# Kernel optimization log

Hardware: AMD Instinct MI355X
Metric: run time of the kernel (lower is better)

## Reference

```python
import jax, jax.numpy as jnp
import numpy as np

VOCAB, EMB, HID, OUT = 50000, 512, 1024, 4
B, T = 128, 256


def setup_inputs() -> dict:
    key = jax.random.key(0)
    ks = jax.random.split(key, 12)
    std0 = 1.0 / np.sqrt(HID)
    u = lambda k, shp, s: jax.random.uniform(k, shp, jnp.float32, -s, s)
    return {
        "fx": jax.random.randint(ks[0], (B, T), 0, VOCAB),
        "emb": jax.random.normal(ks[1], (VOCAB, EMB), jnp.float32),
        "x2h_w0": u(ks[2], (HID, EMB), std0),
        "x2h_b0": u(ks[3], (HID,), std0),
        "h2h_w0": u(ks[4], (HID, HID), std0),
        "h2h_b0": u(ks[5], (HID,), std0),
        "x2h_w1": u(ks[6], (HID, HID), std0),
        "x2h_b1": u(ks[7], (HID,), std0),
        "h2h_w1": u(ks[8], (HID, HID), std0),
        "h2h_b1": u(ks[9], (HID,), std0),
        "fc_w": u(ks[10], (OUT, HID), 1.0 / np.sqrt(HID)),
        "fc_b": u(ks[11], (OUT,), 1.0 / np.sqrt(HID)),
    }


def reference(fx, emb, x2h_w0, x2h_b0, h2h_w0, h2h_b0,
              x2h_w1, x2h_b1, h2h_w1, h2h_b1, fc_w, fc_b):
    x = emb[fx]                      # [B, T, EMB]
    xT = jnp.swapaxes(x, 0, 1)       # [T, B, EMB] for scan over time
    h0 = jnp.zeros((fx.shape[0], HID), jnp.float32)
    h1 = jnp.zeros((fx.shape[0], HID), jnp.float32)

    def step(carry, xt):
        h0, h1 = carry
        # layer 0: tanh(x2h(x_t) + h2h(h0))
        h0 = jnp.tanh(xt @ x2h_w0.T + x2h_b0 + h0 @ h2h_w0.T + h2h_b0)
        # layer 1 consumes the freshly-updated layer-0 hidden (as in the torch loop)
        h1 = jnp.tanh(h0 @ x2h_w1.T + x2h_b1 + h1 @ h2h_w1.T + h2h_b1)
        return (h0, h1), None

    (h0, h1), _ = jax.lax.scan(step, (h0, h1), xT)
    # fc applied to last timestep's top-layer hidden (outs[-1])
    return h1 @ fc_w.T + fc_b        # [B, OUT]
```

## Files before the change

kernel.cpp:

```cpp
#include <hip/hip_runtime.h>
#include <hip/hip_bf16.h>

#define HID   1024
#define EMB   512
#define BATCH 128
#define TT    256
#define OUTN  4
#define BH    (BATCH * HID)

typedef short bf16x8 __attribute__((ext_vector_type(8)));
typedef float f32x4  __attribute__((ext_vector_type(4)));
typedef int   i32x4  __attribute__((ext_vector_type(4)));

__device__ __forceinline__ float bf2f(unsigned short h) {
    return __uint_as_float(((unsigned)h) << 16);
}
__device__ __forceinline__ unsigned short f2bf(float f) {
    unsigned u = __float_as_uint(f);
    u += 0x7FFFu + ((u >> 16) & 1u);
    return (unsigned short)(u >> 16);
}
__device__ __forceinline__ void cvt8(const float* s, unsigned short* d) {
    float4 a = *(const float4*)s, b = *(const float4*)(s + 4);
    unsigned short t[8] = {f2bf(a.x), f2bf(a.y), f2bf(a.z), f2bf(a.w),
                           f2bf(b.x), f2bf(b.y), f2bf(b.z), f2bf(b.w)};
    *(int4*)d = *(const int4*)t;
}
__device__ __forceinline__ bf16x8 pack8(const float* s) {
    float4 a = *(const float4*)s, b = *(const float4*)(s + 4);
    bf16x8 f;
    f[0] = (short)f2bf(a.x); f[1] = (short)f2bf(a.y);
    f[2] = (short)f2bf(a.z); f[3] = (short)f2bf(a.w);
    f[4] = (short)f2bf(b.x); f[5] = (short)f2bf(b.y);
    f[6] = (short)f2bf(b.z); f[7] = (short)f2bf(b.w);
    return f;
}

__global__ __launch_bounds__(256) void wcvt_kernel(
    const float* __restrict__ w, unsigned short* __restrict__ o)
{
    const int i = (blockIdx.x * 256 + threadIdx.x) * 8;
    cvt8(w + i, o + i);
}

__global__ __launch_bounds__(256) void prefx_kernel(
    const int* __restrict__ fx, const float* __restrict__ emb,
    const unsigned short* __restrict__ wx0b, const float* __restrict__ bx0,
    const float* __restrict__ bh0, unsigned short* __restrict__ pre0)
{
    __shared__ __align__(16) unsigned short A[64 * 520];
    const int mtile = blockIdx.x >> 2;
    const int ntile = blockIdx.x & 3;
    const int tid = threadIdx.x;

    {
        const int row = tid >> 2, part = tid & 3;
        const int r = mtile * 64 + row;
        const int t = r >> 7, b = r & 127;
        const int v = fx[b * TT + t];
        const float* src = emb + (size_t)v * EMB + part * 128;
        unsigned short* dst = A + row * 520 + part * 128;
        #pragma unroll
        for (int i = 0; i < 128; i += 8) cvt8(src + i, dst + i);
    }
    __syncthreads();

    const int wave = tid >> 6, lane = tid & 63, q = lane >> 4, nl = lane & 15;
    const int col0 = ntile * 256 + wave * 64;

    f32x4 acc[4][4] = {};
    for (int kc = 0; kc < 16; ++kc) {
        bf16x8 bfr[4], afr[4];
        #pragma unroll
        for (int nt = 0; nt < 4; ++nt)
            bfr[nt] = *(const bf16x8*)(wx0b + (size_t)(col0 + nt * 16 + nl) * EMB + kc * 32 + q * 8);
        #pragma unroll
        for (int mt = 0; mt < 4; ++mt)
            afr[mt] = *(const bf16x8*)(A + (mt * 16 + nl) * 520 + kc * 32 + q * 8);
        #pragma unroll
        for (int mt = 0; mt < 4; ++mt)
            #pragma unroll
            for (int nt = 0; nt < 4; ++nt)
                acc[mt][nt] = __builtin_amdgcn_mfma_f32_16x16x32_bf16(afr[mt], bfr[nt], acc[mt][nt], 0, 0, 0);
    }

    #pragma unroll
    for (int nt = 0; nt < 4; ++nt) {
        const int gc = col0 + nt * 16 + nl;
        const float bias = bx0[gc] + bh0[gc];
        #pragma unroll
        for (int mt = 0; mt < 4; ++mt)
            #pragma unroll
            for (int r = 0; r < 4; ++r) {
                const int grow = mtile * 64 + mt * 16 + q * 4 + r;
                pre0[(size_t)grow * HID + gc] = f2bf(acc[mt][nt][r] + bias);
            }
    }
}

__device__ __forceinline__ void bypass_store16B(unsigned short* dst, i32x4 v) {
    asm volatile("global_store_dwordx4 %0, %1, off sc0 sc1\n\t"
                 "s_waitcnt vmcnt(0)"
                 :: "v"(dst), "v"(v) : "memory");
}

__device__ __forceinline__ void bypass_load8A(const unsigned short* p2, bf16x8 A[8]) {
    asm volatile(
        "global_load_dwordx4 %0, %8, off sc0 sc1\n\t"
        "global_load_dwordx4 %1, %8, off offset:64 sc0 sc1\n\t"
        "global_load_dwordx4 %2, %8, off offset:128 sc0 sc1\n\t"
        "global_load_dwordx4 %3, %8, off offset:192 sc0 sc1\n\t"
        "global_load_dwordx4 %4, %8, off offset:256 sc0 sc1\n\t"
        "global_load_dwordx4 %5, %8, off offset:320 sc0 sc1\n\t"
        "global_load_dwordx4 %6, %8, off offset:384 sc0 sc1\n\t"
        "global_load_dwordx4 %7, %8, off offset:448 sc0 sc1\n\t"
        "s_waitcnt vmcnt(0)"
        : "=&v"(A[0]), "=&v"(A[1]), "=&v"(A[2]), "=&v"(A[3]),
          "=&v"(A[4]), "=&v"(A[5]), "=&v"(A[6]), "=&v"(A[7])
        : "v"(p2) : "memory");
}

__device__ __forceinline__ void bypass_ld8_seq(const unsigned short* p, bf16x8 r[8]) {
    asm volatile(
        "global_load_dwordx4 %0, %8, off sc0 sc1\n\t"
        "global_load_dwordx4 %1, %8, off offset:16 sc0 sc1\n\t"
        "global_load_dwordx4 %2, %8, off offset:32 sc0 sc1\n\t"
        "global_load_dwordx4 %3, %8, off offset:48 sc0 sc1\n\t"
        "global_load_dwordx4 %4, %8, off offset:64 sc0 sc1\n\t"
        "global_load_dwordx4 %5, %8, off offset:80 sc0 sc1\n\t"
        "global_load_dwordx4 %6, %8, off offset:96 sc0 sc1\n\t"
        "global_load_dwordx4 %7, %8, off offset:112 sc0 sc1\n\t"
        "s_waitcnt vmcnt(0)"
        : "=&v"(r[0]), "=&v"(r[1]), "=&v"(r[2]), "=&v"(r[3]),
          "=&v"(r[4]), "=&v"(r[5]), "=&v"(r[6]), "=&v"(r[7])
        : "v"(p) : "memory");
}

__device__ __forceinline__ void cluster_barrier(unsigned* bar, unsigned target) {
    __syncthreads();
    if (threadIdx.x == 0) {
        __hip_atomic_fetch_add(bar, 1u, __ATOMIC_RELAXED, __HIP_MEMORY_SCOPE_AGENT);
        while (__hip_atomic_load(bar, __ATOMIC_RELAXED, __HIP_MEMORY_SCOPE_AGENT) < target)
            __builtin_amdgcn_s_sleep(2);
    }
    __syncthreads();
}

__global__ __launch_bounds__(512) void rnn_step_kernel(
    const unsigned short* __restrict__ pre0,
    const float* __restrict__ whh0,
    const float* __restrict__ wx1,
    const float* __restrict__ whh1,
    const float* __restrict__ bx1,
    const float* __restrict__ bh1,
    const float* __restrict__ fcw,
    const float* __restrict__ fcb,
    unsigned short* __restrict__ h0buf,
    unsigned short* __restrict__ h1buf,
    unsigned* __restrict__ bars,
    float* __restrict__ out)
{
    __shared__ __align__(16) float ldsbuf[22528];
    float* partials = ldsbuf;
    unsigned short* hst0 = (unsigned short*)(ldsbuf + 8704);
    unsigned short* hst1 = (unsigned short*)(ldsbuf + 8704) + 512;
    unsigned short* h0l  = (unsigned short*)(ldsbuf + 9216);
    #define PT(w, t, i) partials[((w) * 4 + (t)) * 272 + (i)]

    const int bid = blockIdx.x;
    const int cluster = bid & 7;
    const int wg = bid >> 3;
    const int r0 = wg * 32;
    const int tid = threadIdx.x;
    const int wave = tid >> 6, lane = tid & 63, q = lane >> 4, nl = lane & 15;

    bf16x8 bw1[2][4], bw2[2][8];
    {
        const int koff1 = wave * 128;
        #pragma unroll
        for (int ct = 0; ct < 2; ++ct)
            #pragma unroll
            for (int j = 0; j < 4; ++j)
                bw1[ct][j] = pack8(whh0 + (size_t)(r0 + ct * 16 + nl) * HID + koff1 + j * 32 + q * 8);
        const float* src2 = (wave < 4) ? wx1 : whh1;
        const int koff2 = (wave & 3) * 256;
        #pragma unroll
        for (int ct = 0; ct < 2; ++ct)
            #pragma unroll
            for (int j = 0; j < 8; ++j)
                bw2[ct][j] = pack8(src2 + (size_t)(r0 + ct * 16 + nl) * HID + koff2 + j * 32 + q * 8);
    }

    const int row_r = tid >> 5;
    const int col_l = tid & 31;
    const int ct_r = (tid >> 4) & 1;
    const float bias1 = bx1[r0 + col_l] + bh1[r0 + col_l];

    const size_t arow = (size_t)(cluster * 16 + nl) * HID + q * 8;
    unsigned barcount = 0;
    unsigned* bar = bars + cluster * 64;

    unsigned short* h0l_w = h0l + nl * 1032 + (wave & 3) * 256 + q * 8;
    const unsigned short* h0l_r = h0l + nl * 1032 + wave * 128 + q * 8;

    {
        const float pv = bf2f(pre0[(size_t)(cluster * 16 + row_r) * HID + r0 + col_l]);
        hst0[row_r * 32 + col_l] = f2bf(tanhf(pv));
        __syncthreads();
        if (wave == 1) {
            const int row = lane >> 2, seg = (lane & 3) * 8;
            i32x4 v = *(const i32x4*)&hst0[row * 32 + seg];
            bypass_store16B(h0buf + (size_t)BH + (size_t)(cluster * 16 + row) * HID + r0 + seg, v);
        }
        cluster_barrier(bar, ++barcount * 32u);
    }

    float pv_cur = bf2f(pre0[(size_t)(BATCH + cluster * 16 + row_r) * HID + r0 + col_l]);

    #pragma unroll 1
    for (int t = 0; t < TT - 1; ++t) {
        const int pin = t & 1;
        const unsigned short* h0_cur = h0buf + (size_t)(pin ^ 1) * BH;
        unsigned short*       h0_nxt = h0buf + (size_t)pin * BH;
        const unsigned short* h1_prv = h1buf + (size_t)pin * BH;
        unsigned short*       h1_new = h1buf + (size_t)(pin ^ 1) * BH;

        const unsigned short* p2 = (wave < 4 ? h0_cur : h1_prv) + arow + (wave & 3) * 256;

        bf16x8 A[8];
        bypass_load8A(p2, A);

        if (wave < 4) {
            #pragma unroll
            for (int j = 0; j < 8; ++j)
                *(bf16x8*)(h0l_w + j * 32) = A[j];
        }

        const int tn = (t + 2 < TT) ? (t + 2) : (TT - 1);
        const float pv_nxt = bf2f(pre0[(size_t)(tn * BATCH + cluster * 16 + row_r) * HID + r0 + col_l]);

        f32x4 d0 = {0.f,0.f,0.f,0.f}, d1 = {0.f,0.f,0.f,0.f};
        #pragma unroll
        for (int j = 0; j < 8; ++j) {
            d0 = __builtin_amdgcn_mfma_f32_16x16x32_bf16(A[j], bw2[0][j], d0, 0,0,0);
            d1 = __builtin_amdgcn_mfma_f32_16x16x32_bf16(A[j], bw2[1][j], d1, 0,0,0);
        }

        __syncthreads();

        f32x4 c0 = {0.f,0.f,0.f,0.f}, c1 = {0.f,0.f,0.f,0.f};
        #pragma unroll
        for (int j = 0; j < 4; ++j) {
            bf16x8 E = *(const bf16x8*)(h0l_r + j * 32);
            c0 = __builtin_amdgcn_mfma_f32_16x16x32_bf16(E, bw1[0][j], c0, 0,0,0);
            c1 = __builtin_amdgcn_mfma_f32_16x16x32_bf16(E, bw1[1][j], c1, 0,0,0);
        }

        #pragma unroll
        for (int r = 0; r < 4; ++r) {
            const int idx = (q * 4 + r) * 17 + nl;
            PT(wave, 0, idx) = d0[r];
            PT(wave, 1, idx) = d1[r];
            PT(wave, 2, idx) = c0[r];
            PT(wave, 3, idx) = c1[r];
        }
        __syncthreads();
        {
            const int idx = row_r * 17 + (col_l & 15);
            float s1 = bias1, s0 = pv_cur;
            #pragma unroll
            for (int w = 0; w < 8; ++w) {
                s1 += PT(w, ct_r, idx);
                s0 += PT(w, 2 + ct_r, idx);
            }
            hst1[row_r * 32 + col_l] = f2bf(tanhf(s1));
            hst0[row_r * 32 + col_l] = f2bf(tanhf(s0));
        }
        __syncthreads();

        if (wave == 0) {
            const int row = lane >> 2, seg = (lane & 3) * 8;
            i32x4 v = *(const i32x4*)&hst1[row * 32 + seg];
            bypass_store16B(h1_new + (size_t)(cluster * 16 + row) * HID + r0 + seg, v);
        } else if (wave == 1) {
            const int row = lane >> 2, seg = (lane & 3) * 8;
            i32x4 v = *(const i32x4*)&hst0[row * 32 + seg];
            bypass_store16B(h0_nxt + (size_t)(cluster * 16 + row) * HID + r0 + seg, v);
        }
        pv_cur = pv_nxt;
        cluster_barrier(bar, ++barcount * 32u);
    }

    {
        const unsigned short* h0_cur = h0buf;
        const unsigned short* h1_prv = h1buf + (size_t)BH;
        unsigned short*       h1_new = h1buf;

        const unsigned short* p2 = (wave < 4 ? h0_cur : h1_prv) + arow + (wave & 3) * 256;

        bf16x8 A[8];
        bypass_load8A(p2, A);

        f32x4 d0 = {0.f,0.f,0.f,0.f}, d1 = {0.f,0.f,0.f,0.f};
        #pragma unroll
        for (int j = 0; j < 8; ++j) {
            d0 = __builtin_amdgcn_mfma_f32_16x16x32_bf16(A[j], bw2[0][j], d0, 0,0,0);
            d1 = __builtin_amdgcn_mfma_f32_16x16x32_bf16(A[j], bw2[1][j], d1, 0,0,0);
        }
        #pragma unroll
        for (int r = 0; r < 4; ++r) {
            const int idx = (q * 4 + r) * 17 + nl;
            PT(wave, 0, idx) = d0[r];
            PT(wave, 1, idx) = d1[r];
        }
        __syncthreads();
        {
            const int idx = row_r * 17 + (col_l & 15);
            float s1 = bias1;
            #pragma unroll
            for (int w = 0; w < 8; ++w) s1 += PT(w, ct_r, idx);
            hst1[row_r * 32 + col_l] = f2bf(tanhf(s1));
        }
        __syncthreads();
        if (wave == 0) {
            const int row = lane >> 2, seg = (lane & 3) * 8;
            i32x4 v = *(const i32x4*)&hst1[row * 32 + seg];
            bypass_store16B(h1_new + (size_t)(cluster * 16 + row) * HID + r0 + seg, v);
        }
        cluster_barrier(bar, ++barcount * 32u);
    }

    if (wg == 0) {
        const int o = tid & 3, row = (tid >> 2) & 15, seg = tid >> 6;
        const unsigned short* hp = h1buf + (size_t)(cluster * 16 + row) * HID + seg * 128;
        const float* wp = fcw + (size_t)o * HID + seg * 128;
        float s = 0.f;
        bf16x8 h8[8];
        #pragma unroll 1
        for (int half = 0; half < 2; ++half) {
            bypass_ld8_seq(hp + half * 64, h8);
            #pragma unroll
            for (int i = 0; i < 8; ++i) {
                const float* w = wp + half * 64 + i * 8;
                #pragma unroll
                for (int e = 0; e < 8; ++e)
                    s += bf2f((unsigned short)h8[i][e]) * w[e];
            }
        }
        float* red = ldsbuf;
        red[tid] = s;
        __syncthreads();
        if (tid < 64) {
            float acc = fcb[o];
            #pragma unroll
            for (int sg = 0; sg < 8; ++sg) acc += red[tid + sg * 64];
            out[(cluster * 16 + row) * OUTN + o] = acc;
        }
    }
    #undef PT
}

extern "C" void kernel_launch(void* const* d_in, const int* in_sizes, int n_in,
                              void* d_out, int out_size, void* d_ws, size_t ws_size,
                              hipStream_t stream) {
    const int*   fx   = (const int*)d_in[0];
    const float* emb  = (const float*)d_in[1];
    const float* wx0  = (const float*)d_in[2];
    const float* bx0  = (const float*)d_in[3];
    const float* whh0 = (const float*)d_in[4];
    const float* bh0  = (const float*)d_in[5];
    const float* wx1  = (const float*)d_in[6];
    const float* bx1  = (const float*)d_in[7];
    const float* whh1 = (const float*)d_in[8];
    const float* bh1  = (const float*)d_in[9];
    const float* fcw  = (const float*)d_in[10];
    const float* fcb  = (const float*)d_in[11];
    float* outp = (float*)d_out;

    char* ws = (char*)d_ws;
    unsigned*       bars  = (unsigned*)ws;
    unsigned short* h0buf = (unsigned short*)(ws + 4096);
    unsigned short* h1buf = (unsigned short*)(ws + 4096 + 524288);
    unsigned short* pre0  = (unsigned short*)(ws + 4096 + 2 * 524288);
    unsigned short* wx0b  = h0buf;

    hipMemsetAsync(ws, 0, 4096, stream);

    wcvt_kernel<<<dim3(256), dim3(256), 0, stream>>>(wx0, wx0b);
    prefx_kernel<<<dim3(2048), dim3(256), 0, stream>>>(fx, emb, wx0b, bx0, bh0, pre0);

    hipMemsetAsync(ws + 4096, 0, 2 * 524288, stream);

    void* kargs[] = {(void*)&pre0, (void*)&whh0, (void*)&wx1, (void*)&whh1,
                     (void*)&bx1, (void*)&bh1, (void*)&fcw, (void*)&fcb,
                     (void*)&h0buf, (void*)&h1buf, (void*)&bars, (void*)&outp};
    hipLaunchCooperativeKernel((void*)rnn_step_kernel, dim3(256), dim3(512),
                               kargs, 0, stream);
}
```

Before: 1.391 ms.

## Halve workgroups to 128, each owning 64 hidden columns with LDS-staged hidden state

Each workgroup now computes 64 output columns instead of 32, so the persistent cooperative grid drops from 256 to 128 blocks and each cluster barrier waits on 16 arrivals instead of 32. Hidden states for both layers are loaded cooperatively with coalesced row loads into LDS and read from there as MFMA fragments. This replaces the earlier per-wave strided global loads. The aim is cheaper per-step barriers and less redundant global traffic. The cost is doubled weight registers per thread (bw1/bw2 grow to 4 column tiles), which raises register pressure and spill risk, plus a larger LDS footprint and more MFMA work per block.

```diff
diff --git a/kernel.cpp b/kernel.cpp
--- a/kernel.cpp
+++ b/kernel.cpp
@@ -98,26 +98,29 @@
     }
 }
 
-__device__ __forceinline__ void bypass_store16B(unsigned short* dst, i32x4 v) {
+__device__ __forceinline__ void bypass_store2x16B(unsigned short* dst, i32x4 v0, i32x4 v1) {
     asm volatile("global_store_dwordx4 %0, %1, off sc0 sc1\n\t"
+                 "global_store_dwordx4 %0, %2, off offset:16 sc0 sc1\n\t"
                  "s_waitcnt vmcnt(0)"
-                 :: "v"(dst), "v"(v) : "memory");
-}
-
-__device__ __forceinline__ void bypass_load8A(const unsigned short* p2, bf16x8 A[8]) {
+                 :: "v"(dst), "v"(v0), "v"(v1) : "memory");
+}
+
+__device__ __forceinline__ void bypass_load8x2(const unsigned short* p0,
+                                               const unsigned short* p1,
+                                               bf16x8 r[8]) {
     asm volatile(
         "global_load_dwordx4 %0, %8, off sc0 sc1\n\t"
-        "global_load_dwordx4 %1, %8, off offset:64 sc0 sc1\n\t"
-        "global_load_dwordx4 %2, %8, off offset:128 sc0 sc1\n\t"
-        "global_load_dwordx4 %3, %8, off offset:192 sc0 sc1\n\t"
-        "global_load_dwordx4 %4, %8, off offset:256 sc0 sc1\n\t"
-        "global_load_dwordx4 %5, %8, off offset:320 sc0 sc1\n\t"
-        "global_load_dwordx4 %6, %8, off offset:384 sc0 sc1\n\t"
-        "global_load_dwordx4 %7, %8, off offset:448 sc0 sc1\n\t"
+        "global_load_dwordx4 %1, %8, off offset:1024 sc0 sc1\n\t"
+        "global_load_dwordx4 %2, %8, off offset:2048 sc0 sc1\n\t"
+        "global_load_dwordx4 %3, %8, off offset:3072 sc0 sc1\n\t"
+        "global_load_dwordx4 %4, %9, off sc0 sc1\n\t"
+        "global_load_dwordx4 %5, %9, off offset:1024 sc0 sc1\n\t"
+        "global_load_dwordx4 %6, %9, off offset:2048 sc0 sc1\n\t"
+        "global_load_dwordx4 %7, %9, off offset:3072 sc0 sc1\n\t"
         "s_waitcnt vmcnt(0)"
-        : "=&v"(A[0]), "=&v"(A[1]), "=&v"(A[2]), "=&v"(A[3]),
-          "=&v"(A[4]), "=&v"(A[5]), "=&v"(A[6]), "=&v"(A[7])
-        : "v"(p2) : "memory");
+        : "=&v"(r[0]), "=&v"(r[1]), "=&v"(r[2]), "=&v"(r[3]),
+          "=&v"(r[4]), "=&v"(r[5]), "=&v"(r[6]), "=&v"(r[7])
+        : "v"(p0), "v"(p1) : "memory");
 }
 
 __device__ __forceinline__ void bypass_ld8_seq(const unsigned short* p, bf16x8 r[8]) {
@@ -160,32 +163,33 @@
     unsigned* __restrict__ bars,
     float* __restrict__ out)
 {
-    __shared__ __align__(16) float ldsbuf[22528];
+    __shared__ __align__(16) float ldsbuf[34432];
     float* partials = ldsbuf;
-    unsigned short* hst0 = (unsigned short*)(ldsbuf + 8704);
-    unsigned short* hst1 = (unsigned short*)(ldsbuf + 8704) + 512;
-    unsigned short* h0l  = (unsigned short*)(ldsbuf + 9216);
-    #define PT(w, t, i) partials[((w) * 4 + (t)) * 272 + (i)]
+    unsigned short* hst0 = (unsigned short*)(ldsbuf + 17408);
+    unsigned short* hst1 = hst0 + 1024;
+    unsigned short* h0l  = (unsigned short*)(ldsbuf + 17920);
+    unsigned short* h1l  = (unsigned short*)(ldsbuf + 26176);
+    #define PT(w, s, i) partials[((w) * 8 + (s)) * 272 + (i)]
 
     const int bid = blockIdx.x;
     const int cluster = bid & 7;
     const int wg = bid >> 3;
-    const int r0 = wg * 32;
+    const int r0 = wg * 64;
     const int tid = threadIdx.x;
     const int wave = tid >> 6, lane = tid & 63, q = lane >> 4, nl = lane & 15;
 
-    bf16x8 bw1[2][4], bw2[2][8];
+    bf16x8 bw1[4][4], bw2[4][8];
     {
         const int koff1 = wave * 128;
         #pragma unroll
-        for (int ct = 0; ct < 2; ++ct)
+        for (int ct = 0; ct < 4; ++ct)
             #pragma unroll
             for (int j = 0; j < 4; ++j)
                 bw1[ct][j] = pack8(whh0 + (size_t)(r0 + ct * 16 + nl) * HID + koff1 + j * 32 + q * 8);
         const float* src2 = (wave < 4) ? wx1 : whh1;
         const int koff2 = (wave & 3) * 256;
         #pragma unroll
-        for (int ct = 0; ct < 2; ++ct)
+        for (int ct = 0; ct < 4; ++ct)
             #pragma unroll
             for (int j = 0; j < 8; ++j)
                 bw2[ct][j] = pack8(src2 + (size_t)(r0 + ct * 16 + nl) * HID + koff2 + j * 32 + q * 8);
@@ -193,29 +197,38 @@
 
     const int row_r = tid >> 5;
     const int col_l = tid & 31;
-    const int ct_r = (tid >> 4) & 1;
-    const float bias1 = bx1[r0 + col_l] + bh1[r0 + col_l];
-
-    const size_t arow = (size_t)(cluster * 16 + nl) * HID + q * 8;
+    const int ct_r = col_l >> 4;
+    const float bias1a = bx1[r0 + col_l] + bh1[r0 + col_l];
+    const float bias1b = bx1[r0 + col_l + 32] + bh1[r0 + col_l + 32];
+
     unsigned barcount = 0;
     unsigned* bar = bars + cluster * 64;
 
-    unsigned short* h0l_w = h0l + nl * 1032 + (wave & 3) * 256 + q * 8;
-    const unsigned short* h0l_r = h0l + nl * 1032 + wave * 128 + q * 8;
+    const size_t stg_g = (size_t)(cluster * 16 + 2 * wave) * HID + lane * 8;
+    unsigned short* l0 = h0l + 2 * wave * 1032 + lane * 8;
+    unsigned short* l1 = h1l + 2 * wave * 1032 + lane * 8;
+
+    const unsigned short* asrc2 = (wave < 4) ? h0l : h1l;
+    const int koff2r = (wave & 3) * 256;
+    const int fragbase = nl * 1032 + q * 8;
 
     {
-        const float pv = bf2f(pre0[(size_t)(cluster * 16 + row_r) * HID + r0 + col_l]);
-        hst0[row_r * 32 + col_l] = f2bf(tanhf(pv));
+        const float pva = bf2f(pre0[(size_t)(cluster * 16 + row_r) * HID + r0 + col_l]);
+        const float pvb = bf2f(pre0[(size_t)(cluster * 16 + row_r) * HID + r0 + col_l + 32]);
+        hst0[row_r * 64 + col_l] = f2bf(tanhf(pva));
+        hst0[row_r * 64 + col_l + 32] = f2bf(tanhf(pvb));
         __syncthreads();
         if (wave == 1) {
-            const int row = lane >> 2, seg = (lane & 3) * 8;
-            i32x4 v = *(const i32x4*)&hst0[row * 32 + seg];
-            bypass_store16B(h0buf + (size_t)BH + (size_t)(cluster * 16 + row) * HID + r0 + seg, v);
-        }
-        cluster_barrier(bar, ++barcount * 32u);
-    }
-
-    float pv_cur = bf2f(pre0[(size_t)(BATCH + cluster * 16 + row_r) * HID + r0 + col_l]);
+            const int row = lane >> 2, sg = (lane & 3) * 16;
+            i32x4 v0 = *(const i32x4*)&hst0[row * 64 + sg];
+            i32x4 v1 = *(const i32x4*)&hst0[row * 64 + sg + 8];
+            bypass_store2x16B(h0buf + (size_t)BH + (size_t)(cluster * 16 + row) * HID + r0 + sg, v0, v1);
+        }
+        cluster_barrier(bar, ++barcount * 16u);
+    }
+
+    float pvA = bf2f(pre0[(size_t)(BATCH + cluster * 16 + row_r) * HID + r0 + col_l]);
+    float pvB = bf2f(pre0[(size_t)(BATCH + cluster * 16 + row_r) * HID + r0 + col_l + 32]);
 
     #pragma unroll 1
     for (int t = 0; t < TT - 1; ++t) {
@@ -225,70 +238,92 @@
         const unsigned short* h1_prv = h1buf + (size_t)pin * BH;
         unsigned short*       h1_new = h1buf + (size_t)(pin ^ 1) * BH;
 
-        const unsigned short* p2 = (wave < 4 ? h0_cur : h1_prv) + arow + (wave & 3) * 256;
-
-        bf16x8 A[8];
-        bypass_load8A(p2, A);
-
-        if (wave < 4) {
-            #pragma unroll
-            for (int j = 0; j < 8; ++j)
-                *(bf16x8*)(h0l_w + j * 32) = A[j];
-        }
+        bf16x8 s[8];
+        bypass_load8x2(h0_cur + stg_g, h1_prv + stg_g, s);
+        *(bf16x8*)(l0)        = s[0];
+        *(bf16x8*)(l0 + 512)  = s[1];
+        *(bf16x8*)(l0 + 1032) = s[2];
+        *(bf16x8*)(l0 + 1544) = s[3];
+        *(bf16x8*)(l1)        = s[4];
+        *(bf16x8*)(l1 + 512)  = s[5];
+        *(bf16x8*)(l1 + 1032) = s[6];
+        *(bf16x8*)(l1 + 1544) = s[7];
 
         const int tn = (t + 2 < TT) ? (t + 2) : (TT - 1);
-        const float pv_nxt = bf2f(pre0[(size_t)(tn * BATCH + cluster * 16 + row_r) * HID + r0 + col_l]);
+        const float pnA = bf2f(pre0[(size_t)(tn * BATCH + cluster * 16 + row_r) * HID + r0 + col_l]);
+        const float pnB = bf2f(pre0[(size_t)(tn * BATCH + cluster * 16 + row_r) * HID + r0 + col_l + 32]);
+
+        __syncthreads();
 
         f32x4 d0 = {0.f,0.f,0.f,0.f}, d1 = {0.f,0.f,0.f,0.f};
+        f32x4 d2 = {0.f,0.f,0.f,0.f}, d3 = {0.f,0.f,0.f,0.f};
         #pragma unroll
         for (int j = 0; j < 8; ++j) {
-            d0 = __builtin_amdgcn_mfma_f32_16x16x32_bf16(A[j], bw2[0][j], d0, 0,0,0);
-            d1 = __builtin_amdgcn_mfma_f32_16x16x32_bf16(A[j], bw2[1][j], d1, 0,0,0);
-        }
-
-        __syncthreads();
-
-        f32x4 c0 = {0.f,0.f,0.f,0.f}, c1 = {0.f,0.f,0.f,0.f};
-        #pragma unroll
-        for (int j = 0; j < 4; ++j) {
-            bf16x8 E = *(const bf16x8*)(h0l_r + j * 32);
-            c0 = __builtin_amdgcn_mfma_f32_16x16x32_bf16(E, bw1[0][j], c0, 0,0,0);
-            c1 = __builtin_amdgcn_mfma_f32_16x16x32_bf16(E, bw1[1][j], c1, 0,0,0);
-        }
-
+            bf16x8 A = *(const bf16x8*)(asrc2 + fragbase + koff2r + j * 32);
+            d0 = __builtin_amdgcn_mfma_f32_16x16x32_bf16(A, bw2[0][j], d0, 0,0,0);
+            d1 = __builtin_amdgcn_mfma_f32_16x16x32_bf16(A, bw2[1][j], d1, 0,0,0);
+            d2 = __builtin_amdgcn_mfma_f32_16x16x32_bf16(A, bw2[2][j], d2, 0,0,0);
+            d3 = __builtin_amdgcn_mfma_f32_16x16x32_bf16(A, bw2[3][j], d3, 0,0,0);
+        }
         #pragma unroll
         for (int r = 0; r < 4; ++r) {
             const int idx = (q * 4 + r) * 17 + nl;
             PT(wave, 0, idx) = d0[r];
             PT(wave, 1, idx) = d1[r];
-            PT(wave, 2, idx) = c0[r];
-            PT(wave, 3, idx) = c1[r];
-        }
-        __syncthreads();
+            PT(wave, 2, idx) = d2[r];
+            PT(wave, 3, idx) = d3[r];
+        }
+
+        f32x4 c0 = {0.f,0.f,0.f,0.f}, c1 = {0.f,0.f,0.f,0.f};
+        f32x4 c2 = {0.f,0.f,0.f,0.f}, c3 = {0.f,0.f,0.f,0.f};
+        #pragma unroll
+        for (int j = 0; j < 4; ++j) {
+            bf16x8 E = *(const bf16x8*)(h0l + fragbase + wave * 128 + j * 32);
+            c0 = __builtin_amdgcn_mfma_f32_16x16x32_bf16(E, bw1[0][j], c0, 0,0,0);
+            c1 = __builtin_amdgcn_mfma_f32_16x16x32_bf16(E, bw1[1][j], c1, 0,0,0);
+            c2 = __builtin_amdgcn_mfma_f32_16x16x32_bf16(E, bw1[2][j], c2, 0,0,0);
+            c3 = __builtin_amdgcn_mfma_f32_16x16x32_bf16(E, bw1[3][j], c3, 0,0,0);
+        }
+        #pragma unroll
+        for (int r = 0; r < 4; ++r) {
+            const int idx = (q * 4 + r) * 17 + nl;
+            PT(wave, 4, idx) = c0[r];
+            PT(wave, 5, idx) = c1[r];
+            PT(wave, 6, idx) = c2[r];
+            PT(wave, 7, idx) = c3[r];
+        }
+        __syncthreads();
+
         {
             const int idx = row_r * 17 + (col_l & 15);
-            float s1 = bias1, s0 = pv_cur;
+            float s1a = bias1a, s1b = bias1b, s0a = pvA, s0b = pvB;
             #pragma unroll
             for (int w = 0; w < 8; ++w) {
-                s1 += PT(w, ct_r, idx);
-                s0 += PT(w, 2 + ct_r, idx);
+                s1a += PT(w, ct_r, idx);
+                s1b += PT(w, 2 + ct_r, idx);
+                s0a += PT(w, 4 + ct_r, idx);
+                s0b += PT(w, 6 + ct_r, idx);
             }
-            hst1[row_r * 32 + col_l] = f2bf(tanhf(s1));
-            hst0[row_r * 32 + col_l] = f2bf(tanhf(s0));
+            hst1[row_r * 64 + col_l]      = f2bf(tanhf(s1a));
+            hst1[row_r * 64 + col_l + 32] = f2bf(tanhf(s1b));
+            hst0[row_r * 64 + col_l]      = f2bf(tanhf(s0a));
+            hst0[row_r * 64 + col_l + 32] = f2bf(tanhf(s0b));
         }
         __syncthreads();
 
         if (wave == 0) {
-            const int row = lane >> 2, seg = (lane & 3) * 8;
-            i32x4 v = *(const i32x4*)&hst1[row * 32 + seg];
-            bypass_store16B(h1_new + (size_t)(cluster * 16 + row) * HID + r0 + seg, v);
+            const int row = lane >> 2, sg = (lane & 3) * 16;
+            i32x4 v0 = *(const i32x4*)&hst1[row * 64 + sg];
+            i32x4 v1 = *(const i32x4*)&hst1[row * 64 + sg + 8];
+            bypass_store2x16B(h1_new + (size_t)(cluster * 16 + row) * HID + r0 + sg, v0, v1);
         } else if (wave == 1) {
-            const int row = lane >> 2, seg = (lane & 3) * 8;
-            i32x4 v = *(const i32x4*)&hst0[row * 32 + seg];
-            bypass_store16B(h0_nxt + (size_t)(cluster * 16 + row) * HID + r0 + seg, v);
-        }
-        pv_cur = pv_nxt;
-        cluster_barrier(bar, ++barcount * 32u);
+            const int row = lane >> 2, sg = (lane & 3) * 16;
+            i32x4 v0 = *(const i32x4*)&hst0[row * 64 + sg];
+            i32x4 v1 = *(const i32x4*)&hst0[row * 64 + sg + 8];
+            bypass_store2x16B(h0_nxt + (size_t)(cluster * 16 + row) * HID + r0 + sg, v0, v1);
+        }
+        pvA = pnA; pvB = pnB;
+        cluster_barrier(bar, ++barcount * 16u);
     }
 
     {
@@ -296,38 +331,56 @@
         const unsigned short* h1_prv = h1buf + (size_t)BH;
         unsigned short*       h1_new = h1buf;
 
-        const unsigned short* p2 = (wave < 4 ? h0_cur : h1_prv) + arow + (wave & 3) * 256;
-
-        bf16x8 A[8];
-        bypass_load8A(p2, A);
+        bf16x8 s[8];
+        bypass_load8x2(h0_cur + stg_g, h1_prv + stg_g, s);
+        *(bf16x8*)(l0)        = s[0];
+        *(bf16x8*)(l0 + 512)  = s[1];
+        *(bf16x8*)(l0 + 1032) = s[2];
+        *(bf16x8*)(l0 + 1544) = s[3];
+        *(bf16x8*)(l1)        = s[4];
+        *(bf16x8*)(l1 + 512)  = s[5];
+        *(bf16x8*)(l1 + 1032) = s[6];
+        *(bf16x8*)(l1 + 1544) = s[7];
+        __syncthreads();
 
         f32x4 d0 = {0.f,0.f,0.f,0.f}, d1 = {0.f,0.f,0.f,0.f};
+        f32x4 d2 = {0.f,0.f,0.f,0.f}, d3 = {0.f,0.f,0.f,0.f};
         #pragma unroll
         for (int j = 0; j < 8; ++j) {
-            d0 = __builtin_amdgcn_mfma_f32_16x16x32_bf16(A[j], bw2[0][j], d0, 0,0,0);
-            d1 = __builtin_amdgcn_mfma_f32_16x16x32_bf16(A[j], bw2[1][j], d1, 0,0,0);
+            bf16x8 A = *(const bf16x8*)(asrc2 + fragbase + koff2r + j * 32);
+            d0 = __builtin_amdgcn_mfma_f32_16x16x32_bf16(A, bw2[0][j], d0, 0,0,0);
+            d1 = __builtin_amdgcn_mfma_f32_16x16x32_bf16(A, bw2[1][j], d1, 0,0,0);
+            d2 = __builtin_amdgcn_mfma_f32_16x16x32_bf16(A, bw2[2][j], d2, 0,0,0);
+            d3 = __builtin_amdgcn_mfma_f32_16x16x32_bf16(A, bw2[3][j], d3, 0,0,0);
         }
         #pragma unroll
         for (int r = 0; r < 4; ++r) {
             const int idx = (q * 4 + r) * 17 + nl;
             PT(wave, 0, idx) = d0[r];
             PT(wave, 1, idx) = d1[r];
+            PT(wave, 2, idx) = d2[r];
+            PT(wave, 3, idx) = d3[r];
         }
         __syncthreads();
         {
             const int idx = row_r * 17 + (col_l & 15);
-            float s1 = bias1;
-            #pragma unroll
-            for (int w = 0; w < 8; ++w) s1 += PT(w, ct_r, idx);
-            hst1[row_r * 32 + col_l] = f2bf(tanhf(s1));
+            float s1a = bias1a, s1b = bias1b;
+            #pragma unroll
+            for (int w = 0; w < 8; ++w) {
+                s1a += PT(w, ct_r, idx);
+                s1b += PT(w, 2 + ct_r, idx);
+            }
+            hst1[row_r * 64 + col_l]      = f2bf(tanhf(s1a));
+            hst1[row_r * 64 + col_l + 32] = f2bf(tanhf(s1b));
         }
         __syncthreads();
         if (wave == 0) {
-            const int row = lane >> 2, seg = (lane & 3) * 8;
-            i32x4 v = *(const i32x4*)&hst1[row * 32 + seg];
-            bypass_store16B(h1_new + (size_t)(cluster * 16 + row) * HID + r0 + seg, v);
-        }
-        cluster_barrier(bar, ++barcount * 32u);
+            const int row = lane >> 2, sg = (lane & 3) * 16;
+            i32x4 v0 = *(const i32x4*)&hst1[row * 64 + sg];
+            i32x4 v1 = *(const i32x4*)&hst1[row * 64 + sg + 8];
+            bypass_store2x16B(h1_new + (size_t)(cluster * 16 + row) * HID + r0 + sg, v0, v1);
+        }
+        cluster_barrier(bar, ++barcount * 16u);
     }
 
     if (wg == 0) {
@@ -394,6 +447,6 @@
     void* kargs[] = {(void*)&pre0, (void*)&whh0, (void*)&wx1, (void*)&whh1,
                      (void*)&bx1, (void*)&bh1, (void*)&fcw, (void*)&fcb,
                      (void*)&h0buf, (void*)&h1buf, (void*)&bars, (void*)&outp};
-    hipLaunchCooperativeKernel((void*)rnn_step_kernel, dim3(256), dim3(512),
+    hipLaunchCooperativeKernel((void*)rnn_step_kernel, dim3(128), dim3(512),
                                kargs, 0, stream);
 }
```

After: 1.402 ms. Within noise of the previous version (+0.7%).
